# Optimization experiments

Measured on AMD Instinct MI355X. Metric: run time of the kernel, lower is better.

The kernel has to match this reference:

```python
import jax, jax.numpy as jnp
import numpy as np

BATCH, IN, HID, OUT = 8192, 1024, 4096, 1000

def _l2norm_rows(w):
    # matches F.normalize(p=2, dim=1) with eps=1e-12
    n = jnp.linalg.norm(w, axis=1, keepdims=True)
    return w / jnp.maximum(n, 1e-12)

def setup_inputs() -> dict:
    key = jax.random.key(0)
    k1, k2, k3 = jax.random.split(key, 3)
    x = jax.random.normal(k1, (BATCH, IN), dtype=jnp.float32)
    kohonen_w = _l2norm_rows(jax.random.normal(k2, (HID, IN), dtype=jnp.float32))
    grossberg_w = _l2norm_rows(jax.random.normal(k3, (OUT, HID), dtype=jnp.float32))
    return {"x": x, "kohonen_w": kohonen_w, "grossberg_w": grossberg_w}

def reference(x, kohonen_w, grossberg_w):
    # x: [B, D]; kohonen_w: [H, D]; grossberg_w: [O, H]
    x2 = jnp.sum(x * x, axis=1, keepdims=True)            # [B, 1]
    w2 = jnp.sum(kohonen_w * kohonen_w, axis=1)           # [H]
    d2 = x2 - 2.0 * (x @ kohonen_w.T) + w2[None, :]       # [B, H]
    winners = jnp.argmin(d2, axis=1)                      # [B] (argmin of dist == argmin of dist^2)
    # one-hot @ grossberg_w.T is exactly a row gather of grossberg_w.T
    output = grossberg_w.T[winners]                       # [B, O]
    return output, winners, x.shape[0]
```

## Files before the change

### kernel.cpp

```cpp
#include <hip/hip_runtime.h>
#include <stdint.h>

#define B_SZ 8192
#define D_SZ 1024
#define H_SZ 4096
#define O_SZ 1000

#define MARGIN 0.0625f

typedef float f32x4 __attribute__((ext_vector_type(4)));
typedef __bf16 bf16x8 __attribute__((ext_vector_type(8)));

static __device__ __forceinline__ uint16_t f2bf(float f) {
  uint32_t u = __float_as_uint(f);
  uint32_t r = (u + 0x7fffu + ((u >> 16) & 1u)) >> 16;
  return (uint16_t)r;
}

__global__ __launch_bounds__(256) void convert_bf16(const float* __restrict__ src,
                                                    ushort4* __restrict__ dst, int n4) {
  int i = blockIdx.x * blockDim.x + threadIdx.x;
  if (i < n4) {
    f32x4 v = reinterpret_cast<const f32x4*>(src)[i];
    ushort4 o;
    o.x = f2bf(v[0]); o.y = f2bf(v[1]); o.z = f2bf(v[2]); o.w = f2bf(v[3]);
    dst[i] = o;
  }
}

__global__ __launch_bounds__(64) void convert_w_w2(const float* __restrict__ w,
                                                   uint16_t* __restrict__ wb,
                                                   double* __restrict__ w2d) {
  const int h = blockIdx.x;
  const int l = threadIdx.x;
  const f32x4* wr = reinterpret_cast<const f32x4*>(w + (size_t)h * D_SZ);
  ushort4* wo = reinterpret_cast<ushort4*>(wb + (size_t)h * D_SZ);
  double s = 0.0;
#pragma unroll
  for (int j = 0; j < 4; ++j) {
    f32x4 v = wr[j * 64 + l];
    s += (double)v[0] * v[0] + (double)v[1] * v[1] + (double)v[2] * v[2] + (double)v[3] * v[3];
    ushort4 o;
    o.x = f2bf(v[0]); o.y = f2bf(v[1]); o.z = f2bf(v[2]); o.w = f2bf(v[3]);
    wo[j * 64 + l] = o;
  }
#pragma unroll
  for (int m = 32; m; m >>= 1) s += __shfl_xor(s, m);
  if (l == 0) w2d[h] = s;
}

__global__ __launch_bounds__(512, 2) void kohonen_gemm256(const uint16_t* __restrict__ xb,
                                                          const uint16_t* __restrict__ wb,
                                                          float* __restrict__ tmax64,
                                                          unsigned long long* __restrict__ tmask64) {
  extern __shared__ char smem[];
  const int tid = threadIdx.x;
  const int lane = tid & 63, wid = tid >> 6;
  const int wm = wid >> 2, wn = wid & 3;
  const int r15 = lane & 15, g = lane >> 4;
  const int xorv = (r15 & 7) << 4;
  const int lr = lane >> 3, lp = lane & 7;

  const int bid = blockIdx.x;
  const int wg = (bid & 7) * 64 + (bid >> 3);
  const int bm = wg >> 4, bn = wg & 15;

  const uint16_t* xrow = xb + (size_t)(bm * 256) * D_SZ;
  const uint16_t* wrow = wb + (size_t)(bn * 256) * D_SZ;

  f32x4 acc[8][4] = {};
  bf16x8 Af[4][2];
  bf16x8 Bf[2][2][2];

  auto stage_a = [&](int a, int sp, int kt) {
#pragma unroll
    for (int j = 0; j < 2; ++j) {
      const int pp = lp ^ lr;
      const int sr = wid * 16 + j * 8 + lr;
      const int mr = (sr < 64) ? (a * 64 + sr) : (128 + a * 64 + (sr - 64));
      const uint16_t* src = xrow + (size_t)mr * D_SZ + kt * 64 + pp * 8;
      __builtin_amdgcn_global_load_lds(
          (const __attribute__((address_space(1))) uint32_t*)src,
          (__attribute__((address_space(3))) uint32_t*)(smem + (sp * 2 + a) * 16384 +
                                                        (wid * 16 + j * 8) * 128),
          16, 0, 0);
    }
  };
  auto stage_b = [&](int b, int sp, int kt) {
#pragma unroll
    for (int j = 0; j < 2; ++j) {
      const int pp = lp ^ lr;
      const int sr = wid * 16 + j * 8 + lr;
      const int mr = (sr >> 5) * 64 + b * 32 + (sr & 31);
      const uint16_t* src = wrow + (size_t)mr * D_SZ + kt * 64 + pp * 8;
      __builtin_amdgcn_global_load_lds(
          (const __attribute__((address_space(1))) uint32_t*)src,
          (__attribute__((address_space(3))) uint32_t*)(smem + 65536 + (sp * 2 + b) * 16384 +
                                                        (wid * 16 + j * 8) * 128),
          16, 0, 0);
    }
  };

#define LDA(QM)                                                                  \
  {                                                                              \
    const char* Abq = smem + rp * 32768 + (QM)*16384;                            \
    _Pragma("unroll") for (int mi = 0; mi < 4; ++mi) {                           \
      const int sr = wm * 64 + mi * 16 + r15;                                    \
      _Pragma("unroll") for (int ks = 0; ks < 2; ++ks)                           \
          Af[mi][ks] = *reinterpret_cast<const bf16x8*>(                         \
              Abq + ((sr * 128 + ks * 64 + g * 16) ^ xorv));                     \
    }                                                                            \
  }
#define LDB(QN)                                                                  \
  {                                                                              \
    const char* Bbq = smem + 65536 + rp * 32768 + (QN)*16384;                    \
    _Pragma("unroll") for (int ni = 0; ni < 2; ++ni) {                           \
      const int sr = wn * 32 + ni * 16 + r15;                                    \
      _Pragma("unroll") for (int ks = 0; ks < 2; ++ks)                           \
          Bf[QN][ni][ks] = *reinterpret_cast<const bf16x8*>(                     \
              Bbq + ((sr * 128 + ks * 64 + g * 16) ^ xorv));                     \
    }                                                                            \
  }
#define MFMAQ(QM, QN)                                                            \
  __builtin_amdgcn_s_setprio(1);                                                 \
  _Pragma("unroll") for (int mi = 0; mi < 4; ++mi)                               \
      _Pragma("unroll") for (int ni = 0; ni < 2; ++ni)                           \
          _Pragma("unroll") for (int ks = 0; ks < 2; ++ks)                       \
              acc[(QM)*4 + mi][(QN)*2 + ni] = __builtin_amdgcn_mfma_f32_16x16x32_bf16( \
                  Af[mi][ks], Bf[QN][ni][ks], acc[(QM)*4 + mi][(QN)*2 + ni], 0, 0, 0); \
  __builtin_amdgcn_s_setprio(0);

  stage_a(0, 0, 0);
  stage_b(0, 0, 0);
  stage_b(1, 0, 0);
  stage_a(1, 0, 0);
  asm volatile("s_waitcnt vmcnt(4)" ::: "memory");
  __builtin_amdgcn_s_barrier();

  for (int t = 0; t < 16; ++t) {
    const int rp = t & 1, sp = rp ^ 1, kt = t + 1;
    const bool pf = (t < 15);
    LDA(0);
    LDB(0);
    if (pf) {
      stage_a(0, sp, kt);
      asm volatile("s_waitcnt vmcnt(4)" ::: "memory");
    } else {
      asm volatile("s_waitcnt vmcnt(0)" ::: "memory");
    }
    __builtin_amdgcn_s_barrier();
    MFMAQ(0, 0);
    __builtin_amdgcn_s_barrier();
    LDB(1);
    if (pf) {
      stage_b(0, sp, kt);
      asm volatile("s_waitcnt vmcnt(4)" ::: "memory");
    }
    __builtin_amdgcn_s_barrier();
    MFMAQ(0, 1);
    __builtin_amdgcn_s_barrier();
    LDA(1);
    if (pf) {
      stage_b(1, sp, kt);
      asm volatile("s_waitcnt vmcnt(4)" ::: "memory");
    }
    __builtin_amdgcn_s_barrier();
    MFMAQ(1, 1);
    __builtin_amdgcn_s_barrier();
    if (pf) {
      stage_a(1, sp, kt);
      asm volatile("s_waitcnt vmcnt(4)" ::: "memory");
    }
    __builtin_amdgcn_s_barrier();
    MFMAQ(1, 0);
    __builtin_amdgcn_s_barrier();
  }

  const int tile = bn * 4 + wn;
#pragma unroll
  for (int m = 0; m < 8; ++m) {
    float v[4];
#pragma unroll
    for (int j = 0; j < 4; ++j)
      v[j] = fmaxf(fmaxf(acc[m][0][j], acc[m][1][j]), fmaxf(acc[m][2][j], acc[m][3][j]));
#pragma unroll
    for (int s = 1; s < 16; s <<= 1) {
#pragma unroll
      for (int j = 0; j < 4; ++j) v[j] = fmaxf(v[j], __shfl_xor(v[j], s));
    }
    unsigned long long mk[4];
#pragma unroll
    for (int j = 0; j < 4; ++j) {
      unsigned long long bmask = 0;
      const float thr = v[j] - MARGIN;
#pragma unroll
      for (int n = 0; n < 4; ++n)
        if (acc[m][n][j] >= thr) bmask |= 1ull << (n * 16 + r15);
      mk[j] = bmask;
    }
#pragma unroll
    for (int s = 1; s < 16; s <<= 1) {
#pragma unroll
      for (int j = 0; j < 4; ++j) mk[j] |= __shfl_xor(mk[j], s);
    }
    if (r15 == 0) {
#pragma unroll
      for (int j = 0; j < 4; ++j) {
        const int row = bm * 256 + wm * 128 + m * 16 + g * 4 + j;
        tmax64[(size_t)row * 64 + tile] = v[j];
        tmask64[(size_t)row * 64 + tile] = mk[j];
      }
    }
  }
}

__global__ __launch_bounds__(64) void rescore2(const float* __restrict__ x,
                                               const float* __restrict__ w,
                                               const double* __restrict__ w2d,
                                               const float* __restrict__ tmax64,
                                               const unsigned long long* __restrict__ tmask64,
                                               int* __restrict__ winners,
                                               float* __restrict__ winners_f) {
  const int row = blockIdx.x;
  const int l = threadIdx.x;

  f32x4 xr[4];
  const f32x4* xp = reinterpret_cast<const f32x4*>(x + (size_t)row * D_SZ);
#pragma unroll
  for (int j = 0; j < 4; ++j) xr[j] = xp[j * 64 + l];

  const float pmax = tmax64[(size_t)row * 64 + l];
  const unsigned long long pmask = tmask64[(size_t)row * 64 + l];
  float M = pmax;
#pragma unroll
  for (int m = 1; m < 64; m <<= 1) M = fmaxf(M, __shfl_xor(M, m));
  const float thr = M - MARGIN;

  double bestS = -1e300;
  int bestI = 0x7fffffff;

  unsigned long long bits = __ballot(pmax >= thr && pmask != 0ull);
  while (bits) {
    const int src = __ffsll(bits) - 1;
    unsigned long long tmask = __shfl(pmask, src);
    const int tile = src;
    while (tmask) {
      const int b = __ffsll(tmask) - 1;
      const int h = tile * 64 + b;
      const f32x4* wp = reinterpret_cast<const f32x4*>(w + (size_t)h * D_SZ);
      double dot = 0.0;
#pragma unroll
      for (int j = 0; j < 4; ++j) {
        f32x4 wv = wp[j * 64 + l];
        dot += (double)xr[j][0] * wv[0] + (double)xr[j][1] * wv[1] +
               (double)xr[j][2] * wv[2] + (double)xr[j][3] * wv[3];
      }
#pragma unroll
      for (int m = 32; m; m >>= 1) dot += __shfl_xor(dot, m);
      const double sc = 2.0 * dot - w2d[h];
      if (sc > bestS || (sc == bestS && h < bestI)) { bestS = sc; bestI = h; }
      tmask &= tmask - 1;
    }
    bits &= bits - 1;
  }

  if (l == 0) { winners[row] = bestI; winners_f[row] = (float)bestI; }
}

__global__ __launch_bounds__(256) void transpose_g(const float* __restrict__ g,
                                                   float* __restrict__ gt) {
  __shared__ float t[32][33];
  const int h0 = blockIdx.x * 32;
  const int o0 = blockIdx.y * 32;
  const int lx = threadIdx.x & 31, ly = threadIdx.x >> 5;
  for (int i = ly; i < 32; i += 8) {
    const int o = o0 + i;
    t[i][lx] = (o < O_SZ) ? g[(size_t)o * H_SZ + (h0 + lx)] : 0.f;
  }
  __syncthreads();
  for (int i = ly; i < 32; i += 8) {
    const int o = o0 + lx;
    if (o < O_SZ) gt[(size_t)(h0 + i) * O_SZ + o] = t[lx][i];
  }
}

__global__ __launch_bounds__(256) void gather_out(const float* __restrict__ gt,
                                                  const int* __restrict__ winners,
                                                  float* __restrict__ out) {
  const int row = blockIdx.x;
  const int wsel = winners[row];
  const f32x4* src = reinterpret_cast<const f32x4*>(gt + (size_t)wsel * O_SZ);
  f32x4* dst = reinterpret_cast<f32x4*>(out + (size_t)row * O_SZ);
  if (threadIdx.x < O_SZ / 4) dst[threadIdx.x] = src[threadIdx.x];
  if (row == 0 && threadIdx.x == 0)
    out[(size_t)B_SZ * O_SZ + B_SZ] = (float)B_SZ;
}

extern "C" void kernel_launch(void* const* d_in, const int* in_sizes, int n_in,
                              void* d_out, int out_size, void* d_ws, size_t ws_size,
                              hipStream_t stream) {
  const float* x  = (const float*)d_in[0];
  const float* kw = (const float*)d_in[1];
  const float* gw = (const float*)d_in[2];
  float* out = (float*)d_out;
  char* ws = (char*)d_ws;

  uint16_t*           xb   = (uint16_t*)(ws);
  uint16_t*           wb   = (uint16_t*)(ws + 16777216);
  float*              tmx  = (float*)   (ws + 25165824);
  unsigned long long* tmk  = (unsigned long long*)(ws + 27262976);
  int*                wins = (int*)     (ws + 31457280);
  double*             w2d  = (double*)  (ws + 31490048);
  float*              gt   = (float*)   (ws);

  convert_bf16<<<(B_SZ * D_SZ / 4 + 255) / 256, 256, 0, stream>>>(x, (ushort4*)xb, B_SZ * D_SZ / 4);
  convert_w_w2<<<H_SZ, 64, 0, stream>>>(kw, wb, w2d);

  static bool attr_set = false;
  if (!attr_set) {
    hipFuncSetAttribute((const void*)kohonen_gemm256,
                        hipFuncAttributeMaxDynamicSharedMemorySize, 131072);
    attr_set = true;
  }
  kohonen_gemm256<<<512, 512, 131072, stream>>>(xb, wb, tmx, tmk);

  rescore2<<<B_SZ, 64, 0, stream>>>(x, kw, w2d, tmx, tmk, wins, out + (size_t)B_SZ * O_SZ);

  dim3 g3(H_SZ / 32, (O_SZ + 31) / 32);
  transpose_g<<<g3, 256, 0, stream>>>(gw, gt);

  gather_out<<<B_SZ, 256, 0, stream>>>(gt, wins, out);
}
```

Measured before the change: 123.3 us.

## Fuse output gather into rescore kernel and drop post-MFMA barriers in GEMM loop

```diff
diff --git a/kernel.cpp b/kernel.cpp
--- a/kernel.cpp
+++ b/kernel.cpp
@@ -150,7 +150,6 @@
     }
     __builtin_amdgcn_s_barrier();
     MFMAQ(0, 0);
-    __builtin_amdgcn_s_barrier();
     LDB(1);
     if (pf) {
       stage_b(0, sp, kt);
@@ -158,7 +157,6 @@
     }
     __builtin_amdgcn_s_barrier();
     MFMAQ(0, 1);
-    __builtin_amdgcn_s_barrier();
     LDA(1);
     if (pf) {
       stage_b(1, sp, kt);
@@ -166,14 +164,12 @@
     }
     __builtin_amdgcn_s_barrier();
     MFMAQ(1, 1);
-    __builtin_amdgcn_s_barrier();
     if (pf) {
       stage_a(1, sp, kt);
       asm volatile("s_waitcnt vmcnt(4)" ::: "memory");
     }
     __builtin_amdgcn_s_barrier();
     MFMAQ(1, 0);
-    __builtin_amdgcn_s_barrier();
   }
 
   const int tile = bn * 4 + wn;
@@ -214,13 +210,14 @@
   }
 }
 
-__global__ __launch_bounds__(64) void rescore2(const float* __restrict__ x,
-                                               const float* __restrict__ w,
-                                               const double* __restrict__ w2d,
-                                               const float* __restrict__ tmax64,
-                                               const unsigned long long* __restrict__ tmask64,
-                                               int* __restrict__ winners,
-                                               float* __restrict__ winners_f) {
+__global__ __launch_bounds__(64) void rescore_gather(const float* __restrict__ x,
+                                                     const float* __restrict__ w,
+                                                     const double* __restrict__ w2d,
+                                                     const float* __restrict__ tmax64,
+                                                     const unsigned long long* __restrict__ tmask64,
+                                                     const float* __restrict__ gt,
+                                                     float* __restrict__ out,
+                                                     float* __restrict__ winners_f) {
   const int row = blockIdx.x;
   const int l = threadIdx.x;
 
@@ -264,7 +261,12 @@
     bits &= bits - 1;
   }
 
-  if (l == 0) { winners[row] = bestI; winners_f[row] = (float)bestI; }
+  if (l == 0) winners_f[row] = (float)bestI;
+  const f32x4* gsrc = reinterpret_cast<const f32x4*>(gt + (size_t)bestI * O_SZ);
+  f32x4* gdst = reinterpret_cast<f32x4*>(out + (size_t)row * O_SZ);
+  for (int i = l; i < O_SZ / 4; i += 64) gdst[i] = gsrc[i];
+  if (row == 0 && l == 0)
+    out[(size_t)B_SZ * O_SZ + B_SZ] = (float)B_SZ;
 }
 
 __global__ __launch_bounds__(256) void transpose_g(const float* __restrict__ g,
@@ -284,18 +286,6 @@
   }
 }
 
-__global__ __launch_bounds__(256) void gather_out(const float* __restrict__ gt,
-                                                  const int* __restrict__ winners,
-                                                  float* __restrict__ out) {
-  const int row = blockIdx.x;
-  const int wsel = winners[row];
-  const f32x4* src = reinterpret_cast<const f32x4*>(gt + (size_t)wsel * O_SZ);
-  f32x4* dst = reinterpret_cast<f32x4*>(out + (size_t)row * O_SZ);
-  if (threadIdx.x < O_SZ / 4) dst[threadIdx.x] = src[threadIdx.x];
-  if (row == 0 && threadIdx.x == 0)
-    out[(size_t)B_SZ * O_SZ + B_SZ] = (float)B_SZ;
-}
-
 extern "C" void kernel_launch(void* const* d_in, const int* in_sizes, int n_in,
                               void* d_out, int out_size, void* d_ws, size_t ws_size,
                               hipStream_t stream) {
@@ -309,8 +299,7 @@
   uint16_t*           wb   = (uint16_t*)(ws + 16777216);
   float*              tmx  = (float*)   (ws + 25165824);
   unsigned long long* tmk  = (unsigned long long*)(ws + 27262976);
-  int*                wins = (int*)     (ws + 31457280);
-  double*             w2d  = (double*)  (ws + 31490048);
+  double*             w2d  = (double*)  (ws + 31457280);
   float*              gt   = (float*)   (ws);
 
   convert_bf16<<<(B_SZ * D_SZ / 4 + 255) / 256, 256, 0, stream>>>(x, (ushort4*)xb, B_SZ * D_SZ / 4);
@@ -324,10 +313,9 @@
   }
   kohonen_gemm256<<<512, 512, 131072, stream>>>(xb, wb, tmx, tmk);
 
-  rescore2<<<B_SZ, 64, 0, stream>>>(x, kw, w2d, tmx, tmk, wins, out + (size_t)B_SZ * O_SZ);
-
   dim3 g3(H_SZ / 32, (O_SZ + 31) / 32);
   transpose_g<<<g3, 256, 0, stream>>>(gw, gt);
 
-  gather_out<<<B_SZ, 256, 0, stream>>>(gt, wins, out);
-}
+  rescore_gather<<<B_SZ, 64, 0, stream>>>(x, kw, w2d, tmx, tmk, gt, out,
+                                          out + (size_t)B_SZ * O_SZ);
+}
```

Result: faster. 118.8 us (-3.7%).
